# Kernel optimization log

Hardware: AMD Instinct MI355X
Metric: run time of the kernel (lower is better)

The kernel has to match this reference:

```python
import jax, jax.numpy as jnp
import numpy as np

REVIEW_RATIO = 0.3  # init kwarg


def setup_inputs() -> dict:
    key = jax.random.key(0)
    k1, k2 = jax.random.split(key)
    N, C = 32768, 1000
    output = jax.random.normal(k1, (N, C), dtype=jnp.float32)
    target = jax.random.randint(k2, (N,), 0, C, dtype=jnp.int64)
    return {"output": output, "target": target}


def reference(output, target):
    # per-sample cross-entropy: -log_softmax(output)[i, target[i]]
    logp = jax.nn.log_softmax(output, axis=-1)               # [N, C]
    ce = -jnp.take_along_axis(logp, target[:, None], axis=-1)[:, 0]  # [N]
    n = ce.shape[0]
    k = int(n * REVIEW_RATIO)
    # descending sort; threshold is the k-th largest loss
    sorted_desc = jnp.sort(ce)[::-1]
    lam = sorted_desc[k]
    # zero out losses strictly below the threshold, then mean over ALL samples
    kept = jnp.where(ce < lam, jnp.zeros_like(ce), ce)
    return kept.mean()
```

## Files before the change

kernel.cpp:

```cpp
#include <hip/hip_runtime.h>
#include <stdint.h>


typedef unsigned int uint32;


__global__ __launch_bounds__(256) void ce_hist_kernel(
    const float* __restrict__ logits, const int* __restrict__ target,
    float* __restrict__ ce, uint32* __restrict__ ghist, int N, int C) {
  __shared__ uint32 lh[8192];
  const int tid = (int)threadIdx.x;
  const int lane = tid & 63;
  const int wid = tid >> 6;

  for (int j = tid; j < 8192; j += 256) lh[j] = 0;
  __syncthreads();

  const float4 NEG = make_float4(-INFINITY, -INFINITY, -INFINITY, -INFINITY);
  const int nv4 = C >> 2;
  const int rbase = (int)blockIdx.x * 64 + wid * 16;

  for (int r = 0; r < 16; ++r) {
    const int row = rbase + r;
    if (row >= N) break;
    const float* rp = logits + (size_t)row * (size_t)C;

    const int t = target[row];
    const float ot = rp[t];

    const float4* rp4 = (const float4*)rp;
    float4 v0 = (lane       < nv4) ? rp4[lane      ] : NEG;
    float4 v1 = (lane +  64 < nv4) ? rp4[lane +  64] : NEG;
    float4 v2 = (lane + 128 < nv4) ? rp4[lane + 128] : NEG;
    float4 v3 = (lane + 192 < nv4) ? rp4[lane + 192] : NEG;

    float m = fmaxf(fmaxf(fmaxf(v0.x, v0.y), fmaxf(v0.z, v0.w)),
                    fmaxf(fmaxf(fmaxf(v1.x, v1.y), fmaxf(v1.z, v1.w)),
                          fmaxf(fmaxf(fmaxf(v2.x, v2.y), fmaxf(v2.z, v2.w)),
                                fmaxf(fmaxf(v3.x, v3.y), fmaxf(v3.z, v3.w)))));
#pragma unroll
    for (int off = 1; off < 64; off <<= 1) m = fmaxf(m, __shfl_xor(m, off));

    float e = __expf(v0.x - m) + __expf(v0.y - m) + __expf(v0.z - m) + __expf(v0.w - m)
            + __expf(v1.x - m) + __expf(v1.y - m) + __expf(v1.z - m) + __expf(v1.w - m)
            + __expf(v2.x - m) + __expf(v2.y - m) + __expf(v2.z - m) + __expf(v2.w - m)
            + __expf(v3.x - m) + __expf(v3.y - m) + __expf(v3.z - m) + __expf(v3.w - m);
#pragma unroll
    for (int off = 1; off < 64; off <<= 1) e += __shfl_xor(e, off);

    if (lane == 0) {
      float cev = fmaxf((m - ot) + __logf(e), 0.0f);
      ce[row] = cev;
      uint32 key = __float_as_uint(cev) >> 17;
      atomicAdd(&lh[key >> 1], (key & 1u) ? 0x10000u : 1u);
    }
  }
  __syncthreads();

  uint32* gh = ghist + (size_t)(blockIdx.x & 7) * 8192;
  for (int j = tid; j < 8192; j += 256) {
    uint32 w = lh[j];
    if (w) atomicAdd(&gh[j], w);
  }
}


__device__ void find_level(uint32* H, uint32* g, uint32 rank, int tid,
                           volatile uint32* sel) {
  uint32 c = 0;
#pragma unroll
  for (int j = 0; j < 8; ++j) {
    uint32 w = H[8 * tid + j];
    c += (w & 0xFFFFu) + (w >> 16);
  }
  g[tid] = c;
  __syncthreads();
  for (int off = 1; off < 1024; off <<= 1) {
    uint32 v = g[tid] + ((tid + off < 1024) ? g[tid + off] : 0u);
    __syncthreads();
    g[tid] = v;
    __syncthreads();
  }
  uint32 SG = (tid + 1 < 1024) ? g[tid + 1] : 0u;
  if (SG <= rank && rank < g[tid]) { sel[0] = (uint32)tid; sel[1] = rank - SG; }
  __syncthreads();
  if (tid == 0) {
    uint32 grp = sel[0], kg = sel[1], acc = 0;
    for (int b = 15; b >= 0; --b) {
      uint32 bin = grp * 16u + (uint32)b;
      uint32 w = H[bin >> 1];
      uint32 cc = (bin & 1u) ? (w >> 16) : (w & 0xFFFFu);
      if (kg < acc + cc) { sel[0] = bin; sel[1] = kg - acc; break; }
      acc += cc;
    }
  }
  __syncthreads();
}

__global__ __launch_bounds__(1024) void select_kernel(
    const float* __restrict__ ce, const uint32* __restrict__ ghist,
    float* __restrict__ out, int N, int k) {
  __shared__ uint32 H[8192];
  __shared__ uint32 Cand[8192];
  __shared__ uint32 g[1024];
  __shared__ uint32 sel[2];
  __shared__ uint32 ccnt;
  __shared__ uint32 cnt16[16];
  __shared__ double wsum[16];
  const int tid = (int)threadIdx.x;
  const int lane = tid & 63;
  const float4* ce4 = (const float4*)ce;
  const int N4 = N >> 2;

  if (tid == 0) ccnt = 0;
  if (tid < 16) cnt16[tid] = 0;

  for (int j = tid; j < 8192; j += 1024) {
    uint32 w = 0;
#pragma unroll
    for (int r = 0; r < 8; ++r) w += ghist[(size_t)r * 8192 + j];
    H[j] = w;
  }
  __syncthreads();

  find_level(H, g, (uint32)k, tid, sel);
  const uint32 K = sel[0];
  const uint32 kr1 = sel[1];
  __syncthreads();

  double acc = 0.0;
  const int iters = (N4 + 1023) / 1024;
  for (int it = 0; it < iters; ++it) {
    int i = it * 1024 + tid;
    float4 x;
    if (i < N4) x = ce4[i];
    else x = make_float4(-1.0f, -1.0f, -1.0f, -1.0f);
    bool valid = (i < N4);
    uint32 u[4];
    float f[4];
    f[0] = x.x; f[1] = x.y; f[2] = x.z; f[3] = x.w;
#pragma unroll
    for (int j = 0; j < 4; ++j) {
      u[j] = __float_as_uint(f[j]);
      uint32 key = u[j] >> 17;
      if (valid && key > K) acc += (double)f[j];
      bool mine = valid && (key == K);
      unsigned long long mk = __ballot(mine);
      uint32 cnt = (uint32)__popcll(mk);
      if (cnt) {
        int src = (int)__ffsll(mk) - 1;
        uint32 base = 0;
        if (lane == src) base = atomicAdd(&ccnt, cnt);
        base = (uint32)__shfl((int)base, src);
        if (mine) {
          uint32 p = base + (uint32)__popcll(mk & ((1ull << lane) - 1ull));
          if (p < 8192u) Cand[p] = u[j];
        }
      }
    }
  }
  __syncthreads();
  const uint32 c = (ccnt < 8192u) ? ccnt : 8192u;

  for (int j = tid; j < 8192; j += 1024) H[j] = 0;
  __syncthreads();
  for (uint32 j = (uint32)tid; j < c; j += 1024u) {
    uint32 key2 = (Cand[j] >> 4) & 0x3FFFu;
    atomicAdd(&H[key2 >> 1], (key2 & 1u) ? 0x10000u : 1u);
  }
  __syncthreads();
  find_level(H, g, kr1, tid, sel);
  const uint32 B2 = sel[0];
  const uint32 kr2 = sel[1];
  __syncthreads();

  const uint32 lam_hi = (K << 17) | (B2 << 4);

  for (uint32 j = (uint32)tid; j < c; j += 1024u) {
    uint32 uj = Cand[j];
    if ((uj >> 4) == (lam_hi >> 4)) atomicAdd(&cnt16[uj & 15u], 1u);
  }
  __syncthreads();
  if (tid == 0) {
    uint32 kg = kr2, accu = 0;
    for (int b = 15; b >= 0; --b) {
      uint32 cc = cnt16[b];
      if (kg < accu + cc) { sel[0] = lam_hi | (uint32)b; break; }
      accu += cc;
    }
  }
  __syncthreads();
  const uint32 lam_u = sel[0];

  for (uint32 j = (uint32)tid; j < c; j += 1024u) {
    uint32 uj = Cand[j];
    if (uj >= lam_u) acc += (double)__uint_as_float(uj);
  }

#pragma unroll
  for (int off = 1; off < 64; off <<= 1) acc += __shfl_xor(acc, off);
  if ((tid & 63) == 0) wsum[tid >> 6] = acc;
  __syncthreads();
  if (tid == 0) {
    double tsum = 0.0;
    for (int i = 0; i < 16; ++i) tsum += wsum[i];
    out[0] = (float)(tsum / (double)N);
  }
}

extern "C" void kernel_launch(void* const* d_in, const int* in_sizes, int n_in,
                              void* d_out, int out_size, void* d_ws, size_t ws_size,
                              hipStream_t stream) {
  const float* logits = (const float*)d_in[0];
  const int* target = (const int*)d_in[1];
  float* out = (float*)d_out;

  const int N = in_sizes[1];
  const int C = in_sizes[0] / N;

  float* ce = (float*)d_ws;
  uint32* ghist = (uint32*)((char*)d_ws + (size_t)N * sizeof(float));

  hipMemsetAsync(ghist, 0, 8 * 8192 * sizeof(uint32), stream);

  int grid = (N + 63) / 64;
  ce_hist_kernel<<<grid, 256, 0, stream>>>(logits, target, ce, ghist, N, C);

  int k = (int)((double)N * 0.3);

  select_kernel<<<1, 1024, 0, stream>>>(ce, ghist, out, N, k);
}
```

Baseline: 224.0 us.

## Fuse CE, histogram and top-k select into one cooperative grid kernel

Replaces the memset, the CE/histogram kernel and the single-block select kernel with one cooperative kernel that uses grid.sync between phases. Per-sample losses stay in shared memory, so the 1024-thread block no longer rescans the full CE array. The global histogram is zeroed inside the kernel and the next row's logits are register-prefetched. The cost is several grid-wide barriers, a cooperative launch of 512 blocks that must all be co-resident, and a fixed 4096-entry candidate capacity per segment with no overflow guard.

```diff
diff --git a/kernel.cpp b/kernel.cpp
--- a/kernel.cpp
+++ b/kernel.cpp
@@ -1,39 +1,102 @@
 #include <hip/hip_runtime.h>
+#include <hip/hip_cooperative_groups.h>
 #include <stdint.h>
 
-
+namespace cg = cooperative_groups;
 typedef unsigned int uint32;
 
 
-__global__ __launch_bounds__(256) void ce_hist_kernel(
+#define TPB 256
+#define ROWS_PER_BLK 64
+#define ROWS_PER_WAVE 16
+#define HWORDS 8192
+#define NREP 8
+#define SEGCAP 4096
+
+__device__ void find_level_256(uint32* H, uint32* g, uint32 rank, int tid,
+                               volatile uint32* sel) {
+  uint32 c = 0;
+#pragma unroll 8
+  for (int j = 0; j < 32; ++j) {
+    uint32 w = H[32 * tid + j];
+    c += (w & 0xFFFFu) + (w >> 16);
+  }
+  g[tid] = c;
+  __syncthreads();
+  for (int off = 1; off < 256; off <<= 1) {
+    uint32 v = g[tid] + ((tid + off < 256) ? g[tid + off] : 0u);
+    __syncthreads();
+    g[tid] = v;
+    __syncthreads();
+  }
+  uint32 SG = (tid + 1 < 256) ? g[tid + 1] : 0u;
+  if (SG <= rank && rank < g[tid]) { sel[0] = (uint32)tid; sel[1] = rank - SG; }
+  __syncthreads();
+  if (tid == 0) {
+    uint32 grp = sel[0], kg = sel[1], acc = 0;
+    for (int b = 63; b >= 0; --b) {
+      uint32 bin = grp * 64u + (uint32)b;
+      uint32 w = H[bin >> 1];
+      uint32 cc = (bin & 1u) ? (w >> 16) : (w & 0xFFFFu);
+      if (kg < acc + cc) { sel[0] = bin; sel[1] = kg - acc; break; }
+      acc += cc;
+    }
+  }
+  __syncthreads();
+}
+
+__global__ __launch_bounds__(TPB, 4) void review_loss_kernel(
     const float* __restrict__ logits, const int* __restrict__ target,
-    float* __restrict__ ce, uint32* __restrict__ ghist, int N, int C) {
-  __shared__ uint32 lh[8192];
+    uint32* __restrict__ rep,
+    uint32* __restrict__ cand,
+    uint32* __restrict__ ccnt,
+    uint32* __restrict__ kkr,
+    double* __restrict__ partials,
+    float* __restrict__ out, int N, int C, int k) {
+  cg::grid_group grid = cg::this_grid();
+  __shared__ uint32 H[HWORDS];
+  __shared__ float stash[ROWS_PER_BLK];
+  __shared__ uint32 g[256];
+  __shared__ uint32 sel[2];
+  __shared__ uint32 cnt8[8];
+  __shared__ double wsum[4];
+
   const int tid = (int)threadIdx.x;
   const int lane = tid & 63;
   const int wid = tid >> 6;
-
-  for (int j = tid; j < 8192; j += 256) lh[j] = 0;
-  __syncthreads();
-
+  const int bid = (int)blockIdx.x;
+  const int nblk = (int)gridDim.x;
+
+  for (int j = bid * TPB + tid; j < NREP * HWORDS; j += nblk * TPB) rep[j] = 0;
+  if (bid == 0 && tid < NREP) ccnt[tid] = 0;
+  for (int j = tid; j < HWORDS; j += TPB) H[j] = 0;
+  __syncthreads();
+
+  const int nv4 = C >> 2;
   const float4 NEG = make_float4(-INFINITY, -INFINITY, -INFINITY, -INFINITY);
-  const int nv4 = C >> 2;
-  const int rbase = (int)blockIdx.x * 64 + wid * 16;
-
-  for (int r = 0; r < 16; ++r) {
+  const int rbase = bid * ROWS_PER_BLK + wid * ROWS_PER_WAVE;
+  const float4* rp4 = (const float4*)(logits + (size_t)rbase * (size_t)C);
+
+  float4 a0 = (lane       < nv4) ? rp4[lane      ] : NEG;
+  float4 a1 = (lane +  64 < nv4) ? rp4[lane +  64] : NEG;
+  float4 a2 = (lane + 128 < nv4) ? rp4[lane + 128] : NEG;
+  float4 a3 = (lane + 192 < nv4) ? rp4[lane + 192] : NEG;
+  int t_next = (rbase < N) ? target[rbase] : 0;
+
+  for (int r = 0; r < ROWS_PER_WAVE; ++r) {
     const int row = rbase + r;
     if (row >= N) break;
-    const float* rp = logits + (size_t)row * (size_t)C;
-
-    const int t = target[row];
-    const float ot = rp[t];
-
-    const float4* rp4 = (const float4*)rp;
-    float4 v0 = (lane       < nv4) ? rp4[lane      ] : NEG;
-    float4 v1 = (lane +  64 < nv4) ? rp4[lane +  64] : NEG;
-    float4 v2 = (lane + 128 < nv4) ? rp4[lane + 128] : NEG;
-    float4 v3 = (lane + 192 < nv4) ? rp4[lane + 192] : NEG;
-
+    float4 v0 = a0, v1 = a1, v2 = a2, v3 = a3;
+    const int t = t_next;
+    const float ot = ((const float*)rp4)[t];
+    if (r + 1 < ROWS_PER_WAVE && row + 1 < N) {
+      const float4* np4 = rp4 + nv4;
+      a0 = (lane       < nv4) ? np4[lane      ] : NEG;
+      a1 = (lane +  64 < nv4) ? np4[lane +  64] : NEG;
+      a2 = (lane + 128 < nv4) ? np4[lane + 128] : NEG;
+      a3 = (lane + 192 < nv4) ? np4[lane + 192] : NEG;
+      t_next = target[row + 1];
+    }
     float m = fmaxf(fmaxf(fmaxf(v0.x, v0.y), fmaxf(v0.z, v0.w)),
                     fmaxf(fmaxf(fmaxf(v1.x, v1.y), fmaxf(v1.z, v1.w)),
                           fmaxf(fmaxf(fmaxf(v2.x, v2.y), fmaxf(v2.z, v2.w)),
@@ -50,161 +113,121 @@
 
     if (lane == 0) {
       float cev = fmaxf((m - ot) + __logf(e), 0.0f);
-      ce[row] = cev;
+      stash[wid * ROWS_PER_WAVE + r] = cev;
       uint32 key = __float_as_uint(cev) >> 17;
-      atomicAdd(&lh[key >> 1], (key & 1u) ? 0x10000u : 1u);
-    }
-  }
-  __syncthreads();
-
-  uint32* gh = ghist + (size_t)(blockIdx.x & 7) * 8192;
-  for (int j = tid; j < 8192; j += 256) {
-    uint32 w = lh[j];
-    if (w) atomicAdd(&gh[j], w);
-  }
-}
-
-
-__device__ void find_level(uint32* H, uint32* g, uint32 rank, int tid,
-                           volatile uint32* sel) {
-  uint32 c = 0;
-#pragma unroll
-  for (int j = 0; j < 8; ++j) {
-    uint32 w = H[8 * tid + j];
-    c += (w & 0xFFFFu) + (w >> 16);
-  }
-  g[tid] = c;
-  __syncthreads();
-  for (int off = 1; off < 1024; off <<= 1) {
-    uint32 v = g[tid] + ((tid + off < 1024) ? g[tid + off] : 0u);
-    __syncthreads();
-    g[tid] = v;
-    __syncthreads();
-  }
-  uint32 SG = (tid + 1 < 1024) ? g[tid + 1] : 0u;
-  if (SG <= rank && rank < g[tid]) { sel[0] = (uint32)tid; sel[1] = rank - SG; }
-  __syncthreads();
-  if (tid == 0) {
-    uint32 grp = sel[0], kg = sel[1], acc = 0;
-    for (int b = 15; b >= 0; --b) {
-      uint32 bin = grp * 16u + (uint32)b;
-      uint32 w = H[bin >> 1];
-      uint32 cc = (bin & 1u) ? (w >> 16) : (w & 0xFFFFu);
-      if (kg < acc + cc) { sel[0] = bin; sel[1] = kg - acc; break; }
-      acc += cc;
-    }
-  }
-  __syncthreads();
-}
-
-__global__ __launch_bounds__(1024) void select_kernel(
-    const float* __restrict__ ce, const uint32* __restrict__ ghist,
-    float* __restrict__ out, int N, int k) {
-  __shared__ uint32 H[8192];
-  __shared__ uint32 Cand[8192];
-  __shared__ uint32 g[1024];
-  __shared__ uint32 sel[2];
-  __shared__ uint32 ccnt;
-  __shared__ uint32 cnt16[16];
-  __shared__ double wsum[16];
-  const int tid = (int)threadIdx.x;
-  const int lane = tid & 63;
-  const float4* ce4 = (const float4*)ce;
-  const int N4 = N >> 2;
-
-  if (tid == 0) ccnt = 0;
-  if (tid < 16) cnt16[tid] = 0;
-
-  for (int j = tid; j < 8192; j += 1024) {
-    uint32 w = 0;
-#pragma unroll
-    for (int r = 0; r < 8; ++r) w += ghist[(size_t)r * 8192 + j];
-    H[j] = w;
-  }
-  __syncthreads();
-
-  find_level(H, g, (uint32)k, tid, sel);
-  const uint32 K = sel[0];
-  const uint32 kr1 = sel[1];
-  __syncthreads();
-
-  double acc = 0.0;
-  const int iters = (N4 + 1023) / 1024;
-  for (int it = 0; it < iters; ++it) {
-    int i = it * 1024 + tid;
-    float4 x;
-    if (i < N4) x = ce4[i];
-    else x = make_float4(-1.0f, -1.0f, -1.0f, -1.0f);
-    bool valid = (i < N4);
-    uint32 u[4];
-    float f[4];
-    f[0] = x.x; f[1] = x.y; f[2] = x.z; f[3] = x.w;
-#pragma unroll
-    for (int j = 0; j < 4; ++j) {
-      u[j] = __float_as_uint(f[j]);
-      uint32 key = u[j] >> 17;
-      if (valid && key > K) acc += (double)f[j];
-      bool mine = valid && (key == K);
-      unsigned long long mk = __ballot(mine);
-      uint32 cnt = (uint32)__popcll(mk);
-      if (cnt) {
-        int src = (int)__ffsll(mk) - 1;
-        uint32 base = 0;
-        if (lane == src) base = atomicAdd(&ccnt, cnt);
-        base = (uint32)__shfl((int)base, src);
-        if (mine) {
-          uint32 p = base + (uint32)__popcll(mk & ((1ull << lane) - 1ull));
-          if (p < 8192u) Cand[p] = u[j];
-        }
-      }
-    }
-  }
-  __syncthreads();
-  const uint32 c = (ccnt < 8192u) ? ccnt : 8192u;
-
-  for (int j = tid; j < 8192; j += 1024) H[j] = 0;
-  __syncthreads();
-  for (uint32 j = (uint32)tid; j < c; j += 1024u) {
-    uint32 key2 = (Cand[j] >> 4) & 0x3FFFu;
-    atomicAdd(&H[key2 >> 1], (key2 & 1u) ? 0x10000u : 1u);
-  }
-  __syncthreads();
-  find_level(H, g, kr1, tid, sel);
-  const uint32 B2 = sel[0];
-  const uint32 kr2 = sel[1];
-  __syncthreads();
-
-  const uint32 lam_hi = (K << 17) | (B2 << 4);
-
-  for (uint32 j = (uint32)tid; j < c; j += 1024u) {
-    uint32 uj = Cand[j];
-    if ((uj >> 4) == (lam_hi >> 4)) atomicAdd(&cnt16[uj & 15u], 1u);
-  }
-  __syncthreads();
-  if (tid == 0) {
-    uint32 kg = kr2, accu = 0;
-    for (int b = 15; b >= 0; --b) {
-      uint32 cc = cnt16[b];
-      if (kg < accu + cc) { sel[0] = lam_hi | (uint32)b; break; }
-      accu += cc;
-    }
-  }
-  __syncthreads();
-  const uint32 lam_u = sel[0];
-
-  for (uint32 j = (uint32)tid; j < c; j += 1024u) {
-    uint32 uj = Cand[j];
-    if (uj >= lam_u) acc += (double)__uint_as_float(uj);
-  }
-
-#pragma unroll
-  for (int off = 1; off < 64; off <<= 1) acc += __shfl_xor(acc, off);
-  if ((tid & 63) == 0) wsum[tid >> 6] = acc;
-  __syncthreads();
-  if (tid == 0) {
-    double tsum = 0.0;
-    for (int i = 0; i < 16; ++i) tsum += wsum[i];
-    out[0] = (float)(tsum / (double)N);
+      atomicAdd(&H[key >> 1], (key & 1u) ? 0x10000u : 1u);
+    }
+    rp4 += nv4;
+  }
+  __syncthreads();
+  grid.sync();
+
+  {
+    uint32* R = rep + (size_t)(bid & 7) * HWORDS;
+    for (int j = tid; j < HWORDS; j += TPB) {
+      uint32 w = H[j];
+      if (w) atomicAdd(&R[j], w);
+    }
+  }
+  grid.sync();
+
+  if (bid == 0) {
+    for (int j = tid; j < HWORDS; j += TPB) {
+      uint32 w = 0;
+#pragma unroll
+      for (int r = 0; r < NREP; ++r) w += rep[(size_t)r * HWORDS + j];
+      H[j] = w;
+    }
+    __syncthreads();
+    find_level_256(H, g, (uint32)k, tid, sel);
+    if (tid == 0) { kkr[0] = sel[0]; kkr[1] = sel[1]; }
+  }
+  grid.sync();
+
+  const uint32 K = kkr[0];
+
+  if (wid == 0) {
+    const int myrow = bid * ROWS_PER_BLK + lane;
+    const bool valid = (myrow < N);
+    const float v = valid ? stash[lane] : 0.0f;
+    const uint32 u = __float_as_uint(v);
+    const uint32 key = u >> 17;
+    double p = (valid && key > K) ? (double)v : 0.0;
+#pragma unroll
+    for (int off = 1; off < 64; off <<= 1) p += __shfl_xor(p, off);
+    if (lane == 0) partials[bid] = p;
+
+    const bool mine = valid && (key == K);
+    unsigned long long mk = __ballot(mine);
+    if (mk) {
+      int src = (int)__ffsll(mk) - 1;
+      uint32 base = 0;
+      if (lane == src) base = atomicAdd(&ccnt[bid & 7], (uint32)__popcll(mk));
+      base = (uint32)__shfl((int)base, src);
+      if (mine) {
+        uint32 pos = base + (uint32)__popcll(mk & ((1ull << lane) - 1ull));
+        cand[(size_t)(bid & 7) * SEGCAP + pos] = u;
+      }
+    }
+  }
+  grid.sync();
+
+  if (bid == 0) {
+    const uint32 kr1 = kkr[1];
+    for (int j = tid; j < HWORDS; j += TPB) H[j] = 0;
+    if (tid < 8) cnt8[tid] = 0;
+    __syncthreads();
+    for (int s = 0; s < NREP; ++s) {
+      const uint32 cs = ccnt[s];
+      for (uint32 j = (uint32)tid; j < cs; j += TPB) {
+        uint32 u = cand[(size_t)s * SEGCAP + j];
+        uint32 k2 = (u >> 3) & 0x3FFFu;
+        atomicAdd(&H[k2 >> 1], (k2 & 1u) ? 0x10000u : 1u);
+      }
+    }
+    __syncthreads();
+    find_level_256(H, g, kr1, tid, sel);
+    const uint32 B2 = sel[0];
+    const uint32 kr2 = sel[1];
+    __syncthreads();
+
+    const uint32 pre = (K << 14) | B2;
+    for (int s = 0; s < NREP; ++s) {
+      const uint32 cs = ccnt[s];
+      for (uint32 j = (uint32)tid; j < cs; j += TPB) {
+        uint32 u = cand[(size_t)s * SEGCAP + j];
+        if ((u >> 3) == pre) atomicAdd(&cnt8[u & 7u], 1u);
+      }
+    }
+    __syncthreads();
+    if (tid == 0) {
+      uint32 kg = kr2, acc = 0;
+      for (int b = 7; b >= 0; --b) {
+        uint32 cc = cnt8[b];
+        if (kg < acc + cc) { sel[0] = (pre << 3) | (uint32)b; break; }
+        acc += cc;
+      }
+    }
+    __syncthreads();
+    const uint32 lam = sel[0];
+
+    double acc = 0.0;
+    for (int j = tid; j < nblk; j += TPB) acc += partials[j];
+    for (int s = 0; s < NREP; ++s) {
+      const uint32 cs = ccnt[s];
+      for (uint32 j = (uint32)tid; j < cs; j += TPB) {
+        uint32 u = cand[(size_t)s * SEGCAP + j];
+        if (u >= lam) acc += (double)__uint_as_float(u);
+      }
+    }
+#pragma unroll
+    for (int off = 1; off < 64; off <<= 1) acc += __shfl_xor(acc, off);
+    if (lane == 0) wsum[wid] = acc;
+    __syncthreads();
+    if (tid == 0) {
+      double tsum = wsum[0] + wsum[1] + wsum[2] + wsum[3];
+      out[0] = (float)(tsum / (double)N);
+    }
   }
 }
 
@@ -215,18 +238,22 @@
   const int* target = (const int*)d_in[1];
   float* out = (float*)d_out;
 
-  const int N = in_sizes[1];
-  const int C = in_sizes[0] / N;
-
-  float* ce = (float*)d_ws;
-  uint32* ghist = (uint32*)((char*)d_ws + (size_t)N * sizeof(float));
-
-  hipMemsetAsync(ghist, 0, 8 * 8192 * sizeof(uint32), stream);
-
-  int grid = (N + 63) / 64;
-  ce_hist_kernel<<<grid, 256, 0, stream>>>(logits, target, ce, ghist, N, C);
-
+  int N = in_sizes[1];
+  int C = in_sizes[0] / N;
   int k = (int)((double)N * 0.3);
 
-  select_kernel<<<1, 1024, 0, stream>>>(ce, ghist, out, N, k);
+  char* p = (char*)d_ws;
+  uint32* rep = (uint32*)p;                       p += (size_t)NREP * HWORDS * 4;
+  uint32* cand = (uint32*)p;                      p += (size_t)NREP * SEGCAP * 4;
+  uint32* ccnt = (uint32*)p;                      p += 64;
+  uint32* kkr = (uint32*)p;                       p += 64;
+  double* partials = (double*)p;
+
+  int nblk = (N + ROWS_PER_BLK - 1) / ROWS_PER_BLK;
+
+  void* args[] = {(void*)&logits, (void*)&target, (void*)&rep, (void*)&cand,
+                  (void*)&ccnt, (void*)&kkr, (void*)&partials, (void*)&out,
+                  (void*)&N, (void*)&C, (void*)&k};
+  hipLaunchCooperativeKernel((const void*)review_loss_kernel, dim3(nblk),
+                             dim3(TPB), args, 0, stream);
 }
```

After: 447.2 us. 99.7% more time.

## Move histogram into select kernel and software-pipeline CE rows with nontemporal loads

Applied to the files above, without the earlier changes.

The CE kernel no longer builds a per-block shared histogram or merges it into global memory with atomics. That removes the 32KB LDS init per block, the global atomic merge and the separate memset. Each wave now handles 4 rows and prefetches the next row's logits with nontemporal loads while reducing the current one, and the grid is larger so more waves are in flight. The single-block select kernel now builds the coarse histogram itself from the CE array with LDS atomics, which adds serial work on one CU. The second-level bin split is also shifted by one bit so the final bucket has 8 entries instead of 16.

```diff
diff --git a/kernel.cpp b/kernel.cpp
--- a/kernel.cpp
+++ b/kernel.cpp
@@ -3,70 +3,94 @@
 
 
 typedef unsigned int uint32;
-
-
-__global__ __launch_bounds__(256) void ce_hist_kernel(
+typedef float vfloat4 __attribute__((ext_vector_type(4)));
+
+#define LDNT(p) __builtin_nontemporal_load(p)
+
+__device__ __forceinline__ float reduce_ce(vfloat4 v0, vfloat4 v1, vfloat4 v2,
+                                           vfloat4 v3, float ot) {
+  float m = fmaxf(fmaxf(fmaxf(v0.x, v0.y), fmaxf(v0.z, v0.w)),
+                  fmaxf(fmaxf(fmaxf(v1.x, v1.y), fmaxf(v1.z, v1.w)),
+                        fmaxf(fmaxf(fmaxf(v2.x, v2.y), fmaxf(v2.z, v2.w)),
+                              fmaxf(fmaxf(v3.x, v3.y), fmaxf(v3.z, v3.w)))));
+#pragma unroll
+  for (int off = 1; off < 64; off <<= 1) m = fmaxf(m, __shfl_xor(m, off));
+  float e = __expf(v0.x - m) + __expf(v0.y - m) + __expf(v0.z - m) + __expf(v0.w - m)
+          + __expf(v1.x - m) + __expf(v1.y - m) + __expf(v1.z - m) + __expf(v1.w - m)
+          + __expf(v2.x - m) + __expf(v2.y - m) + __expf(v2.z - m) + __expf(v2.w - m)
+          + __expf(v3.x - m) + __expf(v3.y - m) + __expf(v3.z - m) + __expf(v3.w - m);
+#pragma unroll
+  for (int off = 1; off < 64; off <<= 1) e += __shfl_xor(e, off);
+  return fmaxf((m - ot) + __logf(e), 0.0f);
+}
+
+__global__ __launch_bounds__(256) void ce_kernel(
     const float* __restrict__ logits, const int* __restrict__ target,
-    float* __restrict__ ce, uint32* __restrict__ ghist, int N, int C) {
-  __shared__ uint32 lh[8192];
-  const int tid = (int)threadIdx.x;
-  const int lane = tid & 63;
-  const int wid = tid >> 6;
-
-  for (int j = tid; j < 8192; j += 256) lh[j] = 0;
-  __syncthreads();
-
-  const float4 NEG = make_float4(-INFINITY, -INFINITY, -INFINITY, -INFINITY);
+    float* __restrict__ ce, int N, int C) {
+  const int lane = (int)(threadIdx.x & 63);
+  const int wave = (int)((blockIdx.x * blockDim.x + threadIdx.x) >> 6);
+  const int r0 = wave * 4;
+  if (r0 >= N) return;
+
   const int nv4 = C >> 2;
-  const int rbase = (int)blockIdx.x * 64 + wid * 16;
-
-  for (int r = 0; r < 16; ++r) {
-    const int row = rbase + r;
-    if (row >= N) break;
-    const float* rp = logits + (size_t)row * (size_t)C;
-
-    const int t = target[row];
-    const float ot = rp[t];
-
-    const float4* rp4 = (const float4*)rp;
-    float4 v0 = (lane       < nv4) ? rp4[lane      ] : NEG;
-    float4 v1 = (lane +  64 < nv4) ? rp4[lane +  64] : NEG;
-    float4 v2 = (lane + 128 < nv4) ? rp4[lane + 128] : NEG;
-    float4 v3 = (lane + 192 < nv4) ? rp4[lane + 192] : NEG;
-
-    float m = fmaxf(fmaxf(fmaxf(v0.x, v0.y), fmaxf(v0.z, v0.w)),
-                    fmaxf(fmaxf(fmaxf(v1.x, v1.y), fmaxf(v1.z, v1.w)),
-                          fmaxf(fmaxf(fmaxf(v2.x, v2.y), fmaxf(v2.z, v2.w)),
-                                fmaxf(fmaxf(v3.x, v3.y), fmaxf(v3.z, v3.w)))));
-#pragma unroll
-    for (int off = 1; off < 64; off <<= 1) m = fmaxf(m, __shfl_xor(m, off));
-
-    float e = __expf(v0.x - m) + __expf(v0.y - m) + __expf(v0.z - m) + __expf(v0.w - m)
-            + __expf(v1.x - m) + __expf(v1.y - m) + __expf(v1.z - m) + __expf(v1.w - m)
-            + __expf(v2.x - m) + __expf(v2.y - m) + __expf(v2.z - m) + __expf(v2.w - m)
-            + __expf(v3.x - m) + __expf(v3.y - m) + __expf(v3.z - m) + __expf(v3.w - m);
-#pragma unroll
-    for (int off = 1; off < 64; off <<= 1) e += __shfl_xor(e, off);
-
-    if (lane == 0) {
-      float cev = fmaxf((m - ot) + __logf(e), 0.0f);
-      ce[row] = cev;
-      uint32 key = __float_as_uint(cev) >> 17;
-      atomicAdd(&lh[key >> 1], (key & 1u) ? 0x10000u : 1u);
-    }
-  }
-  __syncthreads();
-
-  uint32* gh = ghist + (size_t)(blockIdx.x & 7) * 8192;
-  for (int j = tid; j < 8192; j += 256) {
-    uint32 w = lh[j];
-    if (w) atomicAdd(&gh[j], w);
-  }
-}
-
-
-__device__ void find_level(uint32* H, uint32* g, uint32 rank, int tid,
-                           volatile uint32* sel) {
+  const vfloat4 NEG = {-INFINITY, -INFINITY, -INFINITY, -INFINITY};
+  const vfloat4* p0 = (const vfloat4*)(logits + (size_t)r0 * (size_t)C);
+
+#define LOADQ(d0, d1, d2, d3, bp)                          \
+  d0 = (lane       < nv4) ? LDNT((bp) + lane      ) : NEG; \
+  d1 = (lane +  64 < nv4) ? LDNT((bp) + lane +  64) : NEG; \
+  d2 = (lane + 128 < nv4) ? LDNT((bp) + lane + 128) : NEG; \
+  d3 = (lane + 192 < nv4) ? LDNT((bp) + lane + 192) : NEG;
+
+  vfloat4 a0, a1, a2, a3, b0, b1, b2, b3;
+
+  LOADQ(a0, a1, a2, a3, p0);
+  int ta = target[r0];
+  float ota = ((const float*)p0)[ta];
+
+  bool has1 = (r0 + 1 < N);
+  const vfloat4* p1 = p0 + nv4;
+  if (has1) { LOADQ(b0, b1, b2, b3, p1); }
+  int tb = has1 ? target[r0 + 1] : 0;
+  float otb = has1 ? ((const float*)p1)[tb] : 0.0f;
+  {
+    float cev = reduce_ce(a0, a1, a2, a3, ota);
+    if (lane == 0) ce[r0] = cev;
+  }
+  if (!has1) return;
+
+  bool has2 = (r0 + 2 < N);
+  const vfloat4* p2 = p1 + nv4;
+  if (has2) { LOADQ(a0, a1, a2, a3, p2); }
+  ta = has2 ? target[r0 + 2] : 0;
+  ota = has2 ? ((const float*)p2)[ta] : 0.0f;
+  {
+    float cev = reduce_ce(b0, b1, b2, b3, otb);
+    if (lane == 0) ce[r0 + 1] = cev;
+  }
+  if (!has2) return;
+
+  bool has3 = (r0 + 3 < N);
+  const vfloat4* p3 = p2 + nv4;
+  if (has3) { LOADQ(b0, b1, b2, b3, p3); }
+  tb = has3 ? target[r0 + 3] : 0;
+  otb = has3 ? ((const float*)p3)[tb] : 0.0f;
+  {
+    float cev = reduce_ce(a0, a1, a2, a3, ota);
+    if (lane == 0) ce[r0 + 2] = cev;
+  }
+  if (!has3) return;
+
+  {
+    float cev = reduce_ce(b0, b1, b2, b3, otb);
+    if (lane == 0) ce[r0 + 3] = cev;
+  }
+#undef LOADQ
+}
+
+
+__device__ void find_level_1024(uint32* H, uint32* g, uint32 rank, int tid,
+                                volatile uint32* sel) {
   uint32 c = 0;
 #pragma unroll
   for (int j = 0; j < 8; ++j) {
@@ -98,14 +122,13 @@
 }
 
 __global__ __launch_bounds__(1024) void select_kernel(
-    const float* __restrict__ ce, const uint32* __restrict__ ghist,
-    float* __restrict__ out, int N, int k) {
+    const float* __restrict__ ce, float* __restrict__ out, int N, int k) {
   __shared__ uint32 H[8192];
   __shared__ uint32 Cand[8192];
   __shared__ uint32 g[1024];
   __shared__ uint32 sel[2];
   __shared__ uint32 ccnt;
-  __shared__ uint32 cnt16[16];
+  __shared__ uint32 cnt8[8];
   __shared__ double wsum[16];
   const int tid = (int)threadIdx.x;
   const int lane = tid & 63;
@@ -113,17 +136,23 @@
   const int N4 = N >> 2;
 
   if (tid == 0) ccnt = 0;
-  if (tid < 16) cnt16[tid] = 0;
-
-  for (int j = tid; j < 8192; j += 1024) {
-    uint32 w = 0;
-#pragma unroll
-    for (int r = 0; r < 8; ++r) w += ghist[(size_t)r * 8192 + j];
-    H[j] = w;
-  }
-  __syncthreads();
-
-  find_level(H, g, (uint32)k, tid, sel);
+  if (tid < 8) cnt8[tid] = 0;
+  for (int j = tid; j < 8192; j += 1024) H[j] = 0;
+  __syncthreads();
+
+  for (int i = tid; i < N4; i += 1024) {
+    float4 x = ce4[i];
+    uint32 k0 = __float_as_uint(x.x) >> 17;
+    uint32 k1 = __float_as_uint(x.y) >> 17;
+    uint32 k2 = __float_as_uint(x.z) >> 17;
+    uint32 k3 = __float_as_uint(x.w) >> 17;
+    atomicAdd(&H[k0 >> 1], (k0 & 1u) ? 0x10000u : 1u);
+    atomicAdd(&H[k1 >> 1], (k1 & 1u) ? 0x10000u : 1u);
+    atomicAdd(&H[k2 >> 1], (k2 & 1u) ? 0x10000u : 1u);
+    atomicAdd(&H[k3 >> 1], (k3 & 1u) ? 0x10000u : 1u);
+  }
+  __syncthreads();
+  find_level_1024(H, g, (uint32)k, tid, sel);
   const uint32 K = sel[0];
   const uint32 kr1 = sel[1];
   __syncthreads();
@@ -132,29 +161,25 @@
   const int iters = (N4 + 1023) / 1024;
   for (int it = 0; it < iters; ++it) {
     int i = it * 1024 + tid;
-    float4 x;
-    if (i < N4) x = ce4[i];
-    else x = make_float4(-1.0f, -1.0f, -1.0f, -1.0f);
     bool valid = (i < N4);
-    uint32 u[4];
-    float f[4];
-    f[0] = x.x; f[1] = x.y; f[2] = x.z; f[3] = x.w;
+    float4 x = make_float4(0.f, 0.f, 0.f, 0.f);
+    if (valid) x = ce4[i];
+    float f[4] = {x.x, x.y, x.z, x.w};
 #pragma unroll
     for (int j = 0; j < 4; ++j) {
-      u[j] = __float_as_uint(f[j]);
-      uint32 key = u[j] >> 17;
+      uint32 u = __float_as_uint(f[j]);
+      uint32 key = u >> 17;
       if (valid && key > K) acc += (double)f[j];
       bool mine = valid && (key == K);
       unsigned long long mk = __ballot(mine);
-      uint32 cnt = (uint32)__popcll(mk);
-      if (cnt) {
+      if (mk) {
         int src = (int)__ffsll(mk) - 1;
         uint32 base = 0;
-        if (lane == src) base = atomicAdd(&ccnt, cnt);
+        if (lane == src) base = atomicAdd(&ccnt, (uint32)__popcll(mk));
         base = (uint32)__shfl((int)base, src);
         if (mine) {
           uint32 p = base + (uint32)__popcll(mk & ((1ull << lane) - 1ull));
-          if (p < 8192u) Cand[p] = u[j];
+          if (p < 8192u) Cand[p] = u;
         }
       }
     }
@@ -165,36 +190,36 @@
   for (int j = tid; j < 8192; j += 1024) H[j] = 0;
   __syncthreads();
   for (uint32 j = (uint32)tid; j < c; j += 1024u) {
-    uint32 key2 = (Cand[j] >> 4) & 0x3FFFu;
-    atomicAdd(&H[key2 >> 1], (key2 & 1u) ? 0x10000u : 1u);
-  }
-  __syncthreads();
-  find_level(H, g, kr1, tid, sel);
+    uint32 k2 = (Cand[j] >> 3) & 0x3FFFu;
+    atomicAdd(&H[k2 >> 1], (k2 & 1u) ? 0x10000u : 1u);
+  }
+  __syncthreads();
+  find_level_1024(H, g, kr1, tid, sel);
   const uint32 B2 = sel[0];
   const uint32 kr2 = sel[1];
   __syncthreads();
 
-  const uint32 lam_hi = (K << 17) | (B2 << 4);
+  const uint32 lam_hi = (K << 17) | (B2 << 3);
 
   for (uint32 j = (uint32)tid; j < c; j += 1024u) {
-    uint32 uj = Cand[j];
-    if ((uj >> 4) == (lam_hi >> 4)) atomicAdd(&cnt16[uj & 15u], 1u);
+    uint32 u = Cand[j];
+    if ((u >> 3) == (lam_hi >> 3)) atomicAdd(&cnt8[u & 7u], 1u);
   }
   __syncthreads();
   if (tid == 0) {
-    uint32 kg = kr2, accu = 0;
-    for (int b = 15; b >= 0; --b) {
-      uint32 cc = cnt16[b];
-      if (kg < accu + cc) { sel[0] = lam_hi | (uint32)b; break; }
-      accu += cc;
+    uint32 kg = kr2, a2 = 0;
+    for (int b = 7; b >= 0; --b) {
+      uint32 cc = cnt8[b];
+      if (kg < a2 + cc) { sel[0] = lam_hi | (uint32)b; break; }
+      a2 += cc;
     }
   }
   __syncthreads();
-  const uint32 lam_u = sel[0];
+  const uint32 lam = sel[0];
 
   for (uint32 j = (uint32)tid; j < c; j += 1024u) {
-    uint32 uj = Cand[j];
-    if (uj >= lam_u) acc += (double)__uint_as_float(uj);
+    uint32 u = Cand[j];
+    if (u >= lam) acc += (double)__uint_as_float(u);
   }
 
 #pragma unroll
@@ -217,16 +242,12 @@
 
   const int N = in_sizes[1];
   const int C = in_sizes[0] / N;
+  const int k = (int)((double)N * 0.3);
 
   float* ce = (float*)d_ws;
-  uint32* ghist = (uint32*)((char*)d_ws + (size_t)N * sizeof(float));
-
-  hipMemsetAsync(ghist, 0, 8 * 8192 * sizeof(uint32), stream);
-
-  int grid = (N + 63) / 64;
-  ce_hist_kernel<<<grid, 256, 0, stream>>>(logits, target, ce, ghist, N, C);
-
-  int k = (int)((double)N * 0.3);
-
-  select_kernel<<<1, 1024, 0, stream>>>(ce, ghist, out, N, k);
-}
+
+  int nblk = (N + 15) / 16;
+  ce_kernel<<<nblk, 256, 0, stream>>>(logits, target, ce, N, C);
+
+  select_kernel<<<1, 1024, 0, stream>>>(ce, out, N, k);
+}
```

After: 196.7 us. 1.14x faster.
